# Kernel optimization log

Hardware: AMD Instinct MI355X
Metric: run time of the kernel (lower is better)

## Reference

```python
import jax, jax.numpy as jnp
import numpy as np

BSZ, SEQ, DIM, NH = 2, 2048, 2048, 16
HD = DIM // NH  # 128


def setup_inputs() -> dict:
    key = jax.random.key(0)
    ks = jax.random.split(key, 6)
    x = jax.random.normal(ks[0], (BSZ, SEQ, DIM), dtype=jnp.float32)
    # torch Linear weights: [out_features, in_features]
    scale = 1.0 / np.sqrt(DIM)
    wq = jax.random.normal(ks[1], (DIM, DIM), dtype=jnp.float32) * scale
    wk = jax.random.normal(ks[2], (DIM, DIM), dtype=jnp.float32) * scale
    wv = jax.random.normal(ks[3], (DIM, DIM), dtype=jnp.float32) * scale
    wo = jax.random.normal(ks[4], (DIM, DIM), dtype=jnp.float32) * scale
    # RoPE freqs (llama style): theta=10000
    inv_freq = 1.0 / (10000.0 ** (jnp.arange(0, HD, 2, dtype=jnp.float32) / HD))  # [HD//2]
    t = jnp.arange(SEQ, dtype=jnp.float32)
    angles = jnp.outer(t, inv_freq)  # [SEQ, HD//2]
    freqs_cos = jnp.cos(angles)
    freqs_sin = jnp.sin(angles)
    # causal additive mask [SEQ, SEQ]
    mask = jnp.where(jnp.tril(jnp.ones((SEQ, SEQ), dtype=bool)), 0.0, -jnp.inf).astype(jnp.float32)
    return {"x": x, "wq": wq, "wk": wk, "wv": wv, "wo": wo,
            "freqs_cos": freqs_cos, "freqs_sin": freqs_sin, "mask": mask}


def _apply_rope(v, cos, sin):
    # v: [b, s, h, hd]; complex pairs are interleaved (even=real, odd=imag)
    b, s, h, hd = v.shape
    vr = v.reshape(b, s, h, hd // 2, 2)
    v0, v1 = vr[..., 0], vr[..., 1]
    c = cos[None, :, None, :]  # [1, s, 1, hd//2]
    sn = sin[None, :, None, :]
    out = jnp.stack([v0 * c - v1 * sn, v0 * sn + v1 * c], axis=-1)
    return out.reshape(b, s, h, hd)


def reference(x, wq, wk, wv, wo, freqs_cos, freqs_sin, mask):
    b, s, _ = x.shape
    xq = (x @ wq.T).reshape(b, s, NH, HD)
    xk = (x @ wk.T).reshape(b, s, NH, HD)
    xv = (x @ wv.T).reshape(b, s, NH, HD)
    xq = _apply_rope(xq, freqs_cos, freqs_sin)
    xk = _apply_rope(xk, freqs_cos, freqs_sin)
    # [b, h, s, s]
    scores = jnp.einsum('bqhd,bkhd->bhqk', xq, xk) / jnp.sqrt(jnp.float32(HD))
    scores = scores + mask[None, None, :, :]
    probs = jax.nn.softmax(scores.astype(jnp.float32), axis=-1).astype(scores.dtype)
    out = jnp.einsum('bhqk,bkhd->bqhd', probs, xv).reshape(b, s, NH * HD)
    return out @ wo.T
```

## Files before the change

### kernel.cpp

```cpp
#include <hip/hip_runtime.h>
#include <hip/hip_bf16.h>
#include <stdint.h>

typedef __bf16 bf16x8 __attribute__((ext_vector_type(8)));
typedef float f32x4 __attribute__((ext_vector_type(4)));
typedef unsigned short u16;
typedef unsigned int u32;

#define DEVI __device__ __forceinline__

DEVI u16 f2b(float f){ __bf16 h = (__bf16)f; return __builtin_bit_cast(u16, h); }
DEVI float b2f(u16 u){ return (float)__builtin_bit_cast(__bf16, u); }

constexpr int BSZ = 2, SEQ = 2048, DIM = 2048, NH = 16, HD = 128;

#if defined(__has_builtin)
#if __has_builtin(__builtin_amdgcn_global_load_lds)
#define HAVE_ASYNC_LDS 1
#endif
#endif

DEVI void cp16(void* lds, const void* g){
#ifdef HAVE_ASYNC_LDS
  auto gp = (const __attribute__((address_space(1))) u32*)(uintptr_t)g;
  auto lp = (__attribute__((address_space(3))) u32*)(uintptr_t)lds;
  __builtin_amdgcn_global_load_lds(gp, lp, 16, 0, 0);
#else
  *(uint4*)lds = *(const uint4*)g;
#endif
}

__global__ __launch_bounds__(256) void k_convert(
    const float* __restrict__ x, const float* __restrict__ wq,
    const float* __restrict__ wk, const float* __restrict__ wv,
    const float* __restrict__ wo,
    u16* __restrict__ xb, u16* __restrict__ wqkv, u16* __restrict__ wob)
{
  int e = (blockIdx.x * 256 + threadIdx.x) * 4;
  float4 v; u16* dp;
  if (e < 8388608){
    v = *(const float4*)&x[e]; dp = &xb[e];
  } else if (e < 20971520){
    int o = e - 8388608; int sec = o >> 22; int oo = o & 4194303;
    const float* w = (sec == 0) ? wq : ((sec == 1) ? wk : wv);
    v = *(const float4*)&w[oo]; dp = &wqkv[o];
  } else {
    int o = e - 20971520;
    v = *(const float4*)&wo[o]; dp = &wob[o];
  }
  ushort4 r; r.x = f2b(v.x); r.y = f2b(v.y); r.z = f2b(v.z); r.w = f2b(v.w);
  *(ushort4*)dp = r;
}

DEVI void gemm_core_256x128(u16* smem, const u16* __restrict__ A, const u16* __restrict__ B,
                            int tm, int tn, int t, f32x4 (&acc)[4][4])
{
  const int lane = t & 63, l15 = lane & 15, quad = lane >> 4;
  const int wave = t >> 6, wm = wave >> 1, wn = wave & 1;
  const int swr = (l15 & 7) << 3;
  const int rb = t >> 3;
  const int csw = ((t & 7) ^ (rb & 7)) << 3;
  const u16* As0 = A + (size_t)(tm + rb) * DIM + csw;
  const u16* Bs0 = B + (size_t)(tn + rb) * DIM + csw;

  auto STAGE = [&](int kt){
    const int buf = kt & 1;
    const int kb = kt * 64;
    u16* d = &smem[buf * 24576 + t * 8];
    #pragma unroll
    for (int p = 0; p < 4; ++p)
      cp16(d + p * 4096, As0 + (size_t)p * (64 * DIM) + kb);
    #pragma unroll
    for (int p = 0; p < 2; ++p)
      cp16(d + 16384 + p * 4096, Bs0 + (size_t)p * (64 * DIM) + kb);
  };

  STAGE(0);
  #pragma unroll 2
  for (int kt = 0; kt < DIM / 64; ++kt){
    __syncthreads();
    if (kt < DIM / 64 - 1) STAGE(kt + 1);
    const u16* Ab = &smem[(kt & 1) * 24576];
    const u16* Bb = Ab + 16384;
    bf16x8 Af[4][2], Bf[4][2];
    #pragma unroll
    for (int mt = 0; mt < 4; ++mt)
      #pragma unroll
      for (int ks = 0; ks < 2; ++ks)
        Af[mt][ks] = *(const bf16x8*)&Ab[(wm * 64 + mt * 16 + l15) * 64 + ((ks * 32 + quad * 8) ^ swr)];
    #pragma unroll
    for (int nt = 0; nt < 4; ++nt)
      #pragma unroll
      for (int ks = 0; ks < 2; ++ks)
        Bf[nt][ks] = *(const bf16x8*)&Bb[(wn * 64 + nt * 16 + l15) * 64 + ((ks * 32 + quad * 8) ^ swr)];
    #pragma unroll
    for (int c = 0; c < 4; ++c){
      const int mb = (c >> 1) * 2, nb = (c & 1) * 2;
      __builtin_amdgcn_s_setprio(1);
      #pragma unroll
      for (int mi = 0; mi < 2; ++mi)
        #pragma unroll
        for (int ni = 0; ni < 2; ++ni)
          #pragma unroll
          for (int ks = 0; ks < 2; ++ks)
            acc[mb + mi][nb + ni] = __builtin_amdgcn_mfma_f32_16x16x32_bf16(
                Af[mb + mi][ks], Bf[nb + ni][ks], acc[mb + mi][nb + ni], 0, 0, 0);
      __builtin_amdgcn_s_setprio(0);
    }
  }
  __syncthreads();
}

__global__ __launch_bounds__(512, 2) void k_gemm_qkv(
    const u16* __restrict__ A, const u16* __restrict__ W,
    const float* __restrict__ fc, const float* __restrict__ fs,
    u16* __restrict__ Qd, u16* __restrict__ Kd, u16* __restrict__ Vd)
{
  __shared__ __align__(16) u16 smem[49152];
  const int t = threadIdx.x;
  const int wg = blockIdx.x;
  const int id = (wg & 7) * 96 + (wg >> 3);
  const int tm = (id & 15) << 8;
  const int tn = (id >> 4) << 7;
  f32x4 acc[4][4] = {};
  gemm_core_256x128(smem, A, W, tm, tn, t, acc);

  const int lane = t & 63, l15 = lane & 15, quad = lane >> 4;
  const int wave = t >> 6, wm = wave >> 1, wn = wave & 1;
  u16* Cs = smem;
  #pragma unroll
  for (int mt = 0; mt < 4; ++mt)
    #pragma unroll
    for (int nt = 0; nt < 4; ++nt)
      #pragma unroll
      for (int r = 0; r < 4; ++r){
        int rin = wm * 64 + mt * 16 + quad * 4 + r;
        int col = wn * 64 + nt * 16 + l15;
        Cs[rin * 128 + ((col + rin * 8) & 127)] = f2b(acc[mt][nt][r]);
      }
  __syncthreads();

  const int sec = tn >> 11;
  const int hh = (tn & 2047) >> 7;
  u16* dst = (sec == 0) ? Qd : ((sec == 1) ? Kd : Vd);
  const float qs = (sec == 0) ? (0.08838834764831845f * 1.4426950408889634f) : 1.0f;
  const int col0 = (t & 15) * 8;
  #pragma unroll
  for (int jj = 0; jj < 8; ++jj){
    int row = (t >> 4) + jj * 32;
    int m = tm + row;
    int b = m >> 11, s = m & 2047;
    uint4 cv = *(const uint4*)&Cs[row * 128 + ((col0 + row * 8) & 127)];
    const u16* cp = (const u16*)&cv;
    u16 op[8];
    if (sec < 2){
      float4 c4 = *(const float4*)&fc[(size_t)s * 64 + (col0 >> 1)];
      float4 s4 = *(const float4*)&fs[(size_t)s * 64 + (col0 >> 1)];
      float cc[4] = {c4.x*qs, c4.y*qs, c4.z*qs, c4.w*qs};
      float ss[4] = {s4.x*qs, s4.y*qs, s4.z*qs, s4.w*qs};
      #pragma unroll
      for (int p = 0; p < 4; ++p){
        float a = b2f(cp[2*p]), bb = b2f(cp[2*p+1]);
        op[2*p]   = f2b(a*cc[p] - bb*ss[p]);
        op[2*p+1] = f2b(a*ss[p] + bb*cc[p]);
      }
    } else {
      #pragma unroll
      for (int p = 0; p < 8; ++p) op[p] = cp[p];
    }
    *(uint4*)&dst[((size_t)(b*NH + hh)*SEQ + s)*HD + col0] = *(const uint4*)op;
  }
}

__global__ __launch_bounds__(256) void k_vtrans(
    const u16* __restrict__ V, u16* __restrict__ Vt)
{
  __shared__ u16 ts[64*72];
  const int t = threadIdx.x;
  const int st = blockIdx.x, dt = blockIdx.y, bh = blockIdx.z;
  const size_t base  = (size_t)bh * SEQ * HD;
  const size_t baseT = (size_t)bh * HD * SEQ;
  #pragma unroll
  for (int i = 0; i < 2; ++i){
    int s = i*32 + (t>>3), c = t&7;
    *(uint4*)&ts[s*72 + c*8] = *(const uint4*)&V[base + (size_t)(st*64 + s)*HD + dt*64 + c*8];
  }
  __syncthreads();
  #pragma unroll
  for (int i = 0; i < 2; ++i){
    int d = i*32 + (t>>3), sc = t&7;
    u16 tmp[8];
    #pragma unroll
    for (int j = 0; j < 8; ++j) tmp[j] = ts[(sc*8 + j)*72 + d];
    *(uint4*)&Vt[baseT + (size_t)(dt*64 + d)*SEQ + st*64 + sc*8] = *(const uint4*)tmp;
  }
}

__global__ __launch_bounds__(512) void k_flash(
    const u16* __restrict__ Qd, const u16* __restrict__ Kd,
    const u16* __restrict__ Vt, u16* __restrict__ OP0, u16* __restrict__ OP1,
    float* __restrict__ Mp, float* __restrict__ Lp)
{
  __shared__ u16 Ks[64*136];
  __shared__ u16 Vs[128*72];
  __shared__ u16 Ps[8*16*72];

  const int t = threadIdx.x, lane = t & 63, wave = t >> 6;
  const int l15 = lane & 15, quad = lane >> 4;
  const int j = blockIdx.x >> 1, split = blockIdx.x & 1;
  const int h = blockIdx.y, b = blockIdx.z, bh = b*NH + h;
  const size_t base  = (size_t)bh * SEQ * HD;
  const size_t baseT = (size_t)bh * HD * SEQ;
  u16* Psw = &Ps[wave*16*72];
  u16* OPs = split ? OP1 : OP0;
  const int lo = 17*split, hi = lo + 17;
  const int qt0 = j, qt1 = 15 - j;
  const int len0 = 2*qt0 + 2;

  const int krow = t >> 4, kcol = (t & 15) * 8;
  const int vrow = t >> 3, vcol = (t & 7) * 8;

  for (int pass = 0; pass < 2; ++pass){
    const int qt = pass ? qt1 : qt0;
    const int len = 2*qt + 2;
    int kt0 = pass ? (lo - len0) : lo; if (kt0 < 0) kt0 = 0;
    int kt1 = pass ? (hi - len0) : hi; if (kt1 > len) kt1 = len;
    const int qb = qt*128 + wave*16;

    bf16x8 qf[4];
    #pragma unroll
    for (int ks = 0; ks < 4; ++ks)
      qf[ks] = *(const bf16x8*)&Qd[base + (size_t)(qb + l15)*HD + ks*32 + quad*8];

    f32x4 oacc[8] = {};
    float m_s = -1e30f, l_s = 0.f;

    if (kt0 < kt1){
      uint4 kreg[2], vreg[2];
      #pragma unroll
      for (int i = 0; i < 2; ++i){
        kreg[i] = *(const uint4*)&Kd[base + (size_t)(kt0*64 + i*32 + krow)*HD + kcol];
        vreg[i] = *(const uint4*)&Vt[baseT + (size_t)(i*64 + vrow)*SEQ + kt0*64 + vcol];
      }
      for (int kt = kt0; kt < kt1; ++kt){
        __syncthreads();
        #pragma unroll
        for (int i = 0; i < 2; ++i){
          *(uint4*)&Ks[(i*32 + krow)*136 + kcol] = kreg[i];
          *(uint4*)&Vs[(i*64 + vrow)*72 + vcol] = vreg[i];
        }
        __syncthreads();
        if (kt + 1 < kt1){
          #pragma unroll
          for (int i = 0; i < 2; ++i){
            kreg[i] = *(const uint4*)&Kd[base + (size_t)((kt+1)*64 + i*32 + krow)*HD + kcol];
            vreg[i] = *(const uint4*)&Vt[baseT + (size_t)(i*64 + vrow)*SEQ + (kt+1)*64 + vcol];
          }
        }
        if (kt*64 <= qb + 15){
          f32x4 sacc[4] = {};
          #pragma unroll
          for (int ks = 0; ks < 4; ++ks){
            bf16x8 kf[4];
            #pragma unroll
            for (int nk = 0; nk < 4; ++nk)
              kf[nk] = *(const bf16x8*)&Ks[(nk*16 + l15)*136 + ks*32 + quad*8];
            #pragma unroll
            for (int nk = 0; nk < 4; ++nk)
              sacc[nk] = __builtin_amdgcn_mfma_f32_16x16x32_bf16(kf[nk], qf[ks], sacc[nk], 0, 0, 0);
          }
          if (kt*64 + 63 > qb){
            int q = qb + l15;
            #pragma unroll
            for (int nk = 0; nk < 4; ++nk)
              #pragma unroll
              for (int r = 0; r < 4; ++r){
                int key = kt*64 + nk*16 + quad*4 + r;
                if (key > q) sacc[nk][r] = -1e30f;
              }
          }
          float m4[4];
          #pragma unroll
          for (int nk = 0; nk < 4; ++nk)
            m4[nk] = fmaxf(fmaxf(sacc[nk][0], sacc[nk][1]), fmaxf(sacc[nk][2], sacc[nk][3]));
          float rm = fmaxf(fmaxf(m4[0], m4[1]), fmaxf(m4[2], m4[3]));
          rm = fmaxf(rm, __shfl_xor(rm, 16));
          rm = fmaxf(rm, __shfl_xor(rm, 32));
          float mnew = fmaxf(m_s, rm);
          float alpha = exp2f(m_s - mnew);
          m_s = mnew;
          float s4[4];
          #pragma unroll
          for (int nk = 0; nk < 4; ++nk){
            u16 pk[4];
            float p0 = exp2f(sacc[nk][0] - mnew);
            float p1 = exp2f(sacc[nk][1] - mnew);
            float p2 = exp2f(sacc[nk][2] - mnew);
            float p3 = exp2f(sacc[nk][3] - mnew);
            pk[0] = f2b(p0); pk[1] = f2b(p1); pk[2] = f2b(p2); pk[3] = f2b(p3);
            s4[nk] = (p0 + p1) + (p2 + p3);
            *(uint2*)&Psw[l15*72 + nk*16 + quad*4] = *(const uint2*)pk;
          }
          float rs = (s4[0] + s4[1]) + (s4[2] + s4[3]);
          rs += __shfl_xor(rs, 16);
          rs += __shfl_xor(rs, 32);
          l_s = l_s*alpha + rs;
          #pragma unroll
          for (int db = 0; db < 8; ++db)
            #pragma unroll
            for (int r = 0; r < 4; ++r) oacc[db][r] *= alpha;
          #pragma unroll
          for (int k2 = 0; k2 < 2; ++k2){
            bf16x8 pf = *(const bf16x8*)&Psw[l15*72 + k2*32 + quad*8];
            #pragma unroll
            for (int db = 0; db < 8; ++db){
              bf16x8 vf = *(const bf16x8*)&Vs[(db*16 + l15)*72 + k2*32 + quad*8];
              oacc[db] = __builtin_amdgcn_mfma_f32_16x16x32_bf16(vf, pf, oacc[db], 0, 0, 0);
            }
          }
        }
      }
    }
    {
      int s = qb + l15;
      #pragma unroll
      for (int db = 0; db < 8; ++db){
        u16 ok[4];
        #pragma unroll
        for (int r = 0; r < 4; ++r) ok[r] = f2b(oacc[db][r]);
        *(uint2*)&OPs[(((size_t)(b*SEQ + s))*NH + h)*HD + db*16 + quad*4] = *(const uint2*)ok;
      }
      if (quad == 0){
        size_t mi = ((size_t)split*BSZ*NH + bh)*SEQ + s;
        Mp[mi] = m_s;
        Lp[mi] = l_s;
      }
    }
  }
}

__global__ __launch_bounds__(256) void k_combine(
    u16* __restrict__ OP0, const u16* __restrict__ OP1,
    const float* __restrict__ Mp, const float* __restrict__ Lp)
{
  size_t flat = ((size_t)blockIdx.x*256 + threadIdx.x)*8;
  int h = (int)((flat >> 7) & 15);
  int s = (int)((flat >> 11) & 2047);
  int b = (int)(flat >> 22);
  size_t row = ((size_t)(b*NH + h))*SEQ + s;
  const size_t off1 = (size_t)BSZ*NH*SEQ;
  float m0 = Mp[row], l0 = Lp[row];
  float m1 = Mp[row + off1], l1 = Lp[row + off1];
  float m = fmaxf(m0, m1);
  float w0 = exp2f(m0 - m), w1 = exp2f(m1 - m);
  float inv = 1.0f / (w0*l0 + w1*l1);
  uint4 a = *(const uint4*)&OP0[flat];
  uint4 c = *(const uint4*)&OP1[flat];
  const u16* pa = (const u16*)&a;
  const u16* pc = (const u16*)&c;
  u16 o[8];
  #pragma unroll
  for (int i = 0; i < 8; ++i)
    o[i] = f2b((b2f(pa[i])*w0 + b2f(pc[i])*w1) * inv);
  *(uint4*)&OP0[flat] = *(const uint4*)o;
}

__global__ __launch_bounds__(512, 2) void k_gemm_out(
    const u16* __restrict__ A, const u16* __restrict__ W, float* __restrict__ out)
{
  __shared__ __align__(16) u16 smem[49152];
  const int t = threadIdx.x;
  const int wg = blockIdx.x;
  const int id = (wg & 7) * 32 + (wg >> 3);
  const int tm = (id & 15) << 8;
  const int tn = (id >> 4) << 7;
  f32x4 acc[4][4] = {};
  gemm_core_256x128(smem, A, W, tm, tn, t, acc);
  const int lane = t & 63, l15 = lane & 15, quad = lane >> 4;
  const int wave = t >> 6, wm = wave >> 1, wn = wave & 1;
  #pragma unroll
  for (int mt = 0; mt < 4; ++mt)
    #pragma unroll
    for (int nt = 0; nt < 4; ++nt)
      #pragma unroll
      for (int r = 0; r < 4; ++r){
        int row = tm + wm*64 + mt*16 + quad*4 + r;
        int col = tn + wn*64 + nt*16 + l15;
        out[(size_t)row*DIM + col] = acc[mt][nt][r];
      }
}

extern "C" void kernel_launch(void* const* d_in, const int* in_sizes, int n_in,
                              void* d_out, int out_size, void* d_ws, size_t ws_size,
                              hipStream_t stream)
{
  const float* x  = (const float*)d_in[0];
  const float* wq = (const float*)d_in[1];
  const float* wk = (const float*)d_in[2];
  const float* wv = (const float*)d_in[3];
  const float* wo = (const float*)d_in[4];
  const float* fc = (const float*)d_in[5];
  const float* fs = (const float*)d_in[6];
  float* out = (float*)d_out;

  char* ws = (char*)d_ws;
  u16* xb   = (u16*)(ws);
  u16* wqkv = (u16*)(ws + 16777216);
  u16* wob  = (u16*)(ws + 41943040);
  u16* Qr   = (u16*)(ws + 50331648);
  u16* Kr   = (u16*)(ws + 67108864);
  u16* Vr   = (u16*)(ws + 83886080);
  u16* Ob   = (u16*)(ws + 100663296);
  u16* VtT  = xb;
  u16* OP1  = wqkv;
  float* Mp = (float*)(ws + 33554432);
  float* Lp = (float*)(ws + 34078720);

  k_convert <<<24576, 256, 0, stream>>>(x, wq, wk, wv, wo, xb, wqkv, wob);
  k_gemm_qkv<<<768, 512, 0, stream>>>(xb, wqkv, fc, fs, Qr, Kr, Vr);
  k_vtrans  <<<dim3(32, 2, 32), 256, 0, stream>>>(Vr, VtT);
  k_flash   <<<dim3(16, NH, BSZ), 512, 0, stream>>>(Qr, Kr, VtT, Ob, OP1, Mp, Lp);
  k_combine <<<4096, 256, 0, stream>>>(Ob, OP1, Mp, Lp);
  k_gemm_out<<<256, 512, 0, stream>>>(Ob, wob, out);
}
```

Measured before the change: 434.5 us.

## Swizzle flash-attention LDS tiles, remap blocks per XCD, stage output through LDS

Replaces the padded LDS layouts for K, V and P with XOR-swizzled unpadded tiles in one shared buffer, to avoid bank conflicts while shrinking LDS use. Remaps the flat block index so all blocks of one batch-head land on the same XCD, improving L2 reuse of K/V. Raises wave priority around MFMA bursts and stages the output tile through LDS so global stores become full 16-byte row-contiguous writes. This adds an extra barrier and LDS round trip at the end of each pass.

```diff
diff --git a/kernel.cpp b/kernel.cpp
--- a/kernel.cpp
+++ b/kernel.cpp
@@ -201,24 +201,30 @@
     const u16* __restrict__ Vt, u16* __restrict__ OP0, u16* __restrict__ OP1,
     float* __restrict__ Mp, float* __restrict__ Lp)
 {
-  __shared__ u16 Ks[64*136];
-  __shared__ u16 Vs[128*72];
-  __shared__ u16 Ps[8*16*72];
-
+  __shared__ __align__(16) u16 lds[24576];
   const int t = threadIdx.x, lane = t & 63, wave = t >> 6;
   const int l15 = lane & 15, quad = lane >> 4;
-  const int j = blockIdx.x >> 1, split = blockIdx.x & 1;
-  const int h = blockIdx.y, b = blockIdx.z, bh = b*NH + h;
+  const int swz = (l15 & 7) << 3;
+
+  const int flat = blockIdx.x;
+  const int xcd = flat & 7, idx = flat >> 3;
+  const int bh = xcd * 4 + (idx >> 4);
+  const int x = idx & 15;
+  const int b = bh >> 4, h = bh & 15;
+  const int j = x >> 1, split = x & 1;
+
   const size_t base  = (size_t)bh * SEQ * HD;
   const size_t baseT = (size_t)bh * HD * SEQ;
-  u16* Psw = &Ps[wave*16*72];
+  u16* Ks = lds;
+  u16* Vs = lds + 8192;
+  u16* Psw = lds + 16384 + wave * 1024;
   u16* OPs = split ? OP1 : OP0;
   const int lo = 17*split, hi = lo + 17;
   const int qt0 = j, qt1 = 15 - j;
   const int len0 = 2*qt0 + 2;
 
-  const int krow = t >> 4, kcol = (t & 15) * 8;
-  const int vrow = t >> 3, vcol = (t & 7) * 8;
+  const int krow = t >> 4, kslot = t & 15;
+  const int vrow = t >> 3, vslot = t & 7;
 
   for (int pass = 0; pass < 2; ++pass){
     const int qt = pass ? qt1 : qt0;
@@ -239,22 +245,24 @@
       uint4 kreg[2], vreg[2];
       #pragma unroll
       for (int i = 0; i < 2; ++i){
-        kreg[i] = *(const uint4*)&Kd[base + (size_t)(kt0*64 + i*32 + krow)*HD + kcol];
-        vreg[i] = *(const uint4*)&Vt[baseT + (size_t)(i*64 + vrow)*SEQ + kt0*64 + vcol];
+        kreg[i] = *(const uint4*)&Kd[base + (size_t)(kt0*64 + i*32 + krow)*HD + kslot*8];
+        vreg[i] = *(const uint4*)&Vt[baseT + (size_t)(i*64 + vrow)*SEQ + kt0*64 + vslot*8];
       }
       for (int kt = kt0; kt < kt1; ++kt){
         __syncthreads();
         #pragma unroll
         for (int i = 0; i < 2; ++i){
-          *(uint4*)&Ks[(i*32 + krow)*136 + kcol] = kreg[i];
-          *(uint4*)&Vs[(i*64 + vrow)*72 + vcol] = vreg[i];
+          int kr = i*32 + krow;
+          *(uint4*)&Ks[kr*128 + ((kslot*8) ^ ((kr & 7) << 3))] = kreg[i];
+          int vr = i*64 + vrow;
+          *(uint4*)&Vs[vr*64 + ((vslot ^ (vr & 7)) << 3)] = vreg[i];
         }
         __syncthreads();
         if (kt + 1 < kt1){
           #pragma unroll
           for (int i = 0; i < 2; ++i){
-            kreg[i] = *(const uint4*)&Kd[base + (size_t)((kt+1)*64 + i*32 + krow)*HD + kcol];
-            vreg[i] = *(const uint4*)&Vt[baseT + (size_t)(i*64 + vrow)*SEQ + (kt+1)*64 + vcol];
+            kreg[i] = *(const uint4*)&Kd[base + (size_t)((kt+1)*64 + i*32 + krow)*HD + kslot*8];
+            vreg[i] = *(const uint4*)&Vt[baseT + (size_t)(i*64 + vrow)*SEQ + (kt+1)*64 + vslot*8];
           }
         }
         if (kt*64 <= qb + 15){
@@ -264,10 +272,12 @@
             bf16x8 kf[4];
             #pragma unroll
             for (int nk = 0; nk < 4; ++nk)
-              kf[nk] = *(const bf16x8*)&Ks[(nk*16 + l15)*136 + ks*32 + quad*8];
+              kf[nk] = *(const bf16x8*)&Ks[(nk*16 + l15)*128 + ((ks*32 + quad*8) ^ swz)];
+            __builtin_amdgcn_s_setprio(1);
             #pragma unroll
             for (int nk = 0; nk < 4; ++nk)
               sacc[nk] = __builtin_amdgcn_mfma_f32_16x16x32_bf16(kf[nk], qf[ks], sacc[nk], 0, 0, 0);
+            __builtin_amdgcn_s_setprio(0);
           }
           if (kt*64 + 63 > qb){
             int q = qb + l15;
@@ -299,7 +309,7 @@
             float p3 = exp2f(sacc[nk][3] - mnew);
             pk[0] = f2b(p0); pk[1] = f2b(p1); pk[2] = f2b(p2); pk[3] = f2b(p3);
             s4[nk] = (p0 + p1) + (p2 + p3);
-            *(uint2*)&Psw[l15*72 + nk*16 + quad*4] = *(const uint2*)pk;
+            *(uint2*)&Psw[l15*64 + ((nk*16 + quad*4) ^ swz)] = *(const uint2*)pk;
           }
           float rs = (s4[0] + s4[1]) + (s4[2] + s4[3]);
           rs += __shfl_xor(rs, 16);
@@ -311,27 +321,36 @@
             for (int r = 0; r < 4; ++r) oacc[db][r] *= alpha;
           #pragma unroll
           for (int k2 = 0; k2 < 2; ++k2){
-            bf16x8 pf = *(const bf16x8*)&Psw[l15*72 + k2*32 + quad*8];
+            bf16x8 pf = *(const bf16x8*)&Psw[l15*64 + ((k2*32 + quad*8) ^ swz)];
+            __builtin_amdgcn_s_setprio(1);
             #pragma unroll
             for (int db = 0; db < 8; ++db){
-              bf16x8 vf = *(const bf16x8*)&Vs[(db*16 + l15)*72 + k2*32 + quad*8];
+              bf16x8 vf = *(const bf16x8*)&Vs[(db*16 + l15)*64 + ((k2*32 + quad*8) ^ swz)];
               oacc[db] = __builtin_amdgcn_mfma_f32_16x16x32_bf16(vf, pf, oacc[db], 0, 0, 0);
             }
+            __builtin_amdgcn_s_setprio(0);
           }
         }
       }
     }
+    __syncthreads();
     {
-      int s = qb + l15;
+      u16* Osw = lds + wave*2048;
       #pragma unroll
       for (int db = 0; db < 8; ++db){
         u16 ok[4];
         #pragma unroll
         for (int r = 0; r < 4; ++r) ok[r] = f2b(oacc[db][r]);
-        *(uint2*)&OPs[(((size_t)(b*SEQ + s))*NH + h)*HD + db*16 + quad*4] = *(const uint2*)ok;
+        *(uint2*)&Osw[l15*128 + ((db*16 + quad*4) ^ swz)] = *(const uint2*)ok;
+      }
+      #pragma unroll
+      for (int i = 0; i < 4; ++i){
+        int q = i*4 + quad;
+        uint4 v = *(const uint4*)&Osw[q*128 + ((l15*8) ^ ((q & 7) << 3))];
+        *(uint4*)&OPs[(((size_t)(b*SEQ + qb + q))*NH + h)*HD + l15*8] = v;
       }
       if (quad == 0){
-        size_t mi = ((size_t)split*BSZ*NH + bh)*SEQ + s;
+        size_t mi = ((size_t)split*BSZ*NH + bh)*SEQ + (qb + l15);
         Mp[mi] = m_s;
         Lp[mi] = l_s;
       }
@@ -419,7 +438,7 @@
   k_convert <<<24576, 256, 0, stream>>>(x, wq, wk, wv, wo, xb, wqkv, wob);
   k_gemm_qkv<<<768, 512, 0, stream>>>(xb, wqkv, fc, fs, Qr, Kr, Vr);
   k_vtrans  <<<dim3(32, 2, 32), 256, 0, stream>>>(Vr, VtT);
-  k_flash   <<<dim3(16, NH, BSZ), 512, 0, stream>>>(Qr, Kr, VtT, Ob, OP1, Mp, Lp);
+  k_flash   <<<512, 512, 0, stream>>>(Qr, Kr, VtT, Ob, OP1, Mp, Lp);
   k_combine <<<4096, 256, 0, stream>>>(Ob, OP1, Mp, Lp);
   k_gemm_out<<<256, 512, 0, stream>>>(Ob, wob, out);
 }
```

New measurement: 453.0 us. +4.3%, slower.
